# Kernel optimization log

Hardware: AMD Instinct MI355X
Metric: run time of the kernel (lower is better)

## Reference

```python
import jax, jax.numpy as jnp
import numpy as np

# DirectTuckerNet forward (nonnegative=False => sm/relu are identity):
#   out = A @ G @ kron(C, B).T
# where kron(C,B)[k*J+j, r3*R2+r2] = C[k,r3] * B[j,r2].
# Equivalently (same math, avoids materializing the big KR matrix):
#   M = A @ G, reshaped to (I, R3, R2); out[i, k*J+j] = sum_{r3,r2} M[i,r3,r2] C[k,r3] B[j,r2]

I, J, K = 512, 512, 512
R1, R2, R3 = 4, 4, 4

def setup_inputs() -> dict:
    key = jax.random.key(0)
    kA, kB, kC, kG = jax.random.split(key, 4)
    A = jax.random.uniform(kA, (I, R1), dtype=jnp.float32)
    B = jax.random.uniform(kB, (J, R2), dtype=jnp.float32)
    C = jax.random.uniform(kC, (K, R3), dtype=jnp.float32)
    G = jax.random.uniform(kG, (R1, R2 * R3), dtype=jnp.float32)
    return {"A": A, "B": B, "C": C, "G": G}

def reference(A, B, C, G):
    i, r1 = A.shape
    k, r3 = C.shape
    j, r2 = B.shape
    # M = A @ G : (I, R2*R3); G's flat column axis pairs with kron(C,B)'s (r3, r2) column order
    M = (A @ G).reshape(i, r3, r2)  # (I, R3, R2)
    # out[i, k, j] = sum_{p,q} M[i,p,q] * C[k,p] * B[j,q]
    out = jnp.einsum('ipq,kp,jq->ikj', M, C, B)  # (I, K, J)
    return out.reshape(i, k * j)
```

## Files before the change

kernel.cpp:

```cpp
#include <hip/hip_runtime.h>


#define J_DIM 512

__global__ __launch_bounds__(256) void tucker_fwd(
    const float* __restrict__ A, const float* __restrict__ B,
    const float* __restrict__ C, const float* __restrict__ G,
    float* __restrict__ out)
{
    const int tid = threadIdx.x;
    const int jlane = tid & 31;
    const int rslot = tid >> 5;
    const int rowBase = blockIdx.x * 64;
    const int i = rowBase >> 9;

    const float4* B4 = reinterpret_cast<const float4*>(B);
    float4 b[4][4];
#pragma unroll
    for (int s = 0; s < 4; ++s) {
        const int j0 = s * 128 + jlane * 4;
#pragma unroll
        for (int e = 0; e < 4; ++e) b[s][e] = B4[j0 + e];
    }

    const float4 a = reinterpret_cast<const float4*>(A)[i];
    float W[16];
#pragma unroll
    for (int c = 0; c < 16; ++c)
        W[c] = a.x * G[c] + a.y * G[16 + c] + a.z * G[32 + c] + a.w * G[48 + c];

    const float4* C4 = reinterpret_cast<const float4*>(C);
#pragma unroll
    for (int rr = 0; rr < 8; ++rr) {
        const int row = rowBase + rslot * 8 + rr;
        const int k = row & 511;
        const float4 ck = C4[k];
        const float v0 = ck.x * W[0] + ck.y * W[4] + ck.z * W[8]  + ck.w * W[12];
        const float v1 = ck.x * W[1] + ck.y * W[5] + ck.z * W[9]  + ck.w * W[13];
        const float v2 = ck.x * W[2] + ck.y * W[6] + ck.z * W[10] + ck.w * W[14];
        const float v3 = ck.x * W[3] + ck.y * W[7] + ck.z * W[11] + ck.w * W[15];

        float4* orow = reinterpret_cast<float4*>(out + (size_t)row * J_DIM);
#pragma unroll
        for (int s = 0; s < 4; ++s) {
            float4 o;
            o.x = v0 * b[s][0].x + v1 * b[s][0].y + v2 * b[s][0].z + v3 * b[s][0].w;
            o.y = v0 * b[s][1].x + v1 * b[s][1].y + v2 * b[s][1].z + v3 * b[s][1].w;
            o.z = v0 * b[s][2].x + v1 * b[s][2].y + v2 * b[s][2].z + v3 * b[s][2].w;
            o.w = v0 * b[s][3].x + v1 * b[s][3].y + v2 * b[s][3].z + v3 * b[s][3].w;
            orow[s * 32 + jlane] = o;
        }
    }
}

extern "C" void kernel_launch(void* const* d_in, const int* in_sizes, int n_in,
                              void* d_out, int out_size, void* d_ws, size_t ws_size,
                              hipStream_t stream) {
    const float* A = (const float*)d_in[0];
    const float* B = (const float*)d_in[1];
    const float* C = (const float*)d_in[2];
    const float* G = (const float*)d_in[3];
    float* out = (float*)d_out;

    tucker_fwd<<<4096, 256, 0, stream>>>(A, B, C, G, out);
}
```

Baseline: 98.97 us.

## Remap threads to full-row stores with nontemporal writes and fewer registers

Each thread now covers one float4 column slice across 32 consecutive rows instead of four slices across 8 rows, so 128 threads write a full 2KB row together. The per-thread B cache shrinks from 16 to 4 float4 values and launch bounds ask for higher occupancy. Output stores use nontemporal builtins to avoid polluting cache on a 512MB streaming write. Work per thread still goes through a loop unrolled by 2, so there is more loop overhead and per-row C loads.

```diff
diff --git a/kernel.cpp b/kernel.cpp
--- a/kernel.cpp
+++ b/kernel.cpp
@@ -3,25 +3,24 @@
 
 #define J_DIM 512
 
-__global__ __launch_bounds__(256) void tucker_fwd(
+typedef float f32x4 __attribute__((ext_vector_type(4)));
+
+__global__ __launch_bounds__(256, 8) void tucker_fwd(
     const float* __restrict__ A, const float* __restrict__ B,
     const float* __restrict__ C, const float* __restrict__ G,
     float* __restrict__ out)
 {
     const int tid = threadIdx.x;
-    const int jlane = tid & 31;
-    const int rslot = tid >> 5;
+    const int jlane = tid & 127;
+    const int rslot = tid >> 7;
     const int rowBase = blockIdx.x * 64;
     const int i = rowBase >> 9;
 
     const float4* B4 = reinterpret_cast<const float4*>(B);
-    float4 b[4][4];
-#pragma unroll
-    for (int s = 0; s < 4; ++s) {
-        const int j0 = s * 128 + jlane * 4;
-#pragma unroll
-        for (int e = 0; e < 4; ++e) b[s][e] = B4[j0 + e];
-    }
+    float4 b0 = B4[jlane * 4 + 0];
+    float4 b1 = B4[jlane * 4 + 1];
+    float4 b2 = B4[jlane * 4 + 2];
+    float4 b3 = B4[jlane * 4 + 3];
 
     const float4 a = reinterpret_cast<const float4*>(A)[i];
     float W[16];
@@ -30,26 +29,23 @@
         W[c] = a.x * G[c] + a.y * G[16 + c] + a.z * G[32 + c] + a.w * G[48 + c];
 
     const float4* C4 = reinterpret_cast<const float4*>(C);
-#pragma unroll
-    for (int rr = 0; rr < 8; ++rr) {
-        const int row = rowBase + rslot * 8 + rr;
-        const int k = row & 511;
-        const float4 ck = C4[k];
+    const int row0 = rowBase + rslot * 32;
+    f32x4* obase = reinterpret_cast<f32x4*>(out + (size_t)row0 * J_DIM) + jlane;
+
+#pragma unroll 2
+    for (int rr = 0; rr < 32; ++rr) {
+        const float4 ck = C4[(row0 + rr) & 511];
         const float v0 = ck.x * W[0] + ck.y * W[4] + ck.z * W[8]  + ck.w * W[12];
         const float v1 = ck.x * W[1] + ck.y * W[5] + ck.z * W[9]  + ck.w * W[13];
         const float v2 = ck.x * W[2] + ck.y * W[6] + ck.z * W[10] + ck.w * W[14];
         const float v3 = ck.x * W[3] + ck.y * W[7] + ck.z * W[11] + ck.w * W[15];
 
-        float4* orow = reinterpret_cast<float4*>(out + (size_t)row * J_DIM);
-#pragma unroll
-        for (int s = 0; s < 4; ++s) {
-            float4 o;
-            o.x = v0 * b[s][0].x + v1 * b[s][0].y + v2 * b[s][0].z + v3 * b[s][0].w;
-            o.y = v0 * b[s][1].x + v1 * b[s][1].y + v2 * b[s][1].z + v3 * b[s][1].w;
-            o.z = v0 * b[s][2].x + v1 * b[s][2].y + v2 * b[s][2].z + v3 * b[s][2].w;
-            o.w = v0 * b[s][3].x + v1 * b[s][3].y + v2 * b[s][3].z + v3 * b[s][3].w;
-            orow[s * 32 + jlane] = o;
-        }
+        f32x4 o;
+        o.x = v0 * b0.x + v1 * b0.y + v2 * b0.z + v3 * b0.w;
+        o.y = v0 * b1.x + v1 * b1.y + v2 * b1.z + v3 * b1.w;
+        o.z = v0 * b2.x + v1 * b2.y + v2 * b2.z + v3 * b2.w;
+        o.w = v0 * b3.x + v1 * b3.y + v2 * b3.z + v3 * b3.w;
+        __builtin_nontemporal_store(o, obase + (size_t)rr * 128);
     }
 }
 
```

Result: slower. 103.4 us (+4.4%).
